# Performance work log

Hardware: AMD Instinct MI355X
Metric: run time of the kernel (lower is better)

## Reference

```python
import jax, jax.numpy as jnp
import numpy as np

N_TOTAL = 32768   # sphere points
N0 = 8192         # stage-0 nodes
N1 = 1024         # stage-1/2 nodes per branch
K = 8             # neighbors
C_IN, C_H = 128, 64
COS_T = 0.999     # NMS angular suppression threshold (~2.5 deg)
NEG = -1e30


def setup_inputs():
    key = jax.random.key(0)
    ks = jax.random.split(key, 32)
    f32 = jnp.float32
    def w(k, shape):
        return jax.random.normal(k, shape, f32) * 0.05
    feat_sphere = jax.random.normal(ks[0], (C_IN, N_TOTAL), f32)
    xyz = jax.random.normal(ks[1], (N_TOTAL, 3), f32)
    xyz = xyz / jnp.linalg.norm(xyz, axis=1, keepdims=True)
    inp = {"feat_sphere": feat_sphere, "xyz": xyz}
    for i, nm in enumerate(["0", "1", "2"]):
        inp["ws" + nm] = w(ks[2 + 2 * i], (C_H, C_IN))
        inp["bs" + nm] = w(ks[3 + 2 * i], (C_H,))
    for i, nm in enumerate(["0", "1", "2"]):
        b = 8 + 5 * i
        inp["dg" + nm + "_Wself"] = w(ks[b], (4, C_H, C_H))
        inp["dg" + nm + "_Wnb"] = w(ks[b + 1], (4, C_H, C_H))
        inp["dg" + nm + "_b"] = w(ks[b + 2], (4, C_H))
        inp["dg" + nm + "_head"] = w(ks[b + 3], (C_H,))
        inp["dg" + nm + "_hb"] = w(ks[b + 4], (1,))
    center0 = jnp.repeat(jnp.arange(N0, dtype=jnp.int32), K)
    nb0 = jax.random.randint(ks[24], (N0 * K,), 0, N0)
    inp["edge0"] = jnp.stack([center0, nb0])
    inp["ind0"] = jax.random.randint(ks[25], (N0,), 0, N_TOTAL)
    inp["ind1_scale"] = jax.random.randint(ks[26], (N_TOTAL, N1), 0, N_TOTAL)
    inp["ind2_scale"] = jax.random.randint(ks[27], (N_TOTAL, N1), 0, N_TOTAL)
    return inp


def _dgcn(x, center, neighbor, Wself, Wnb, bias, head, hb, n):
    # x: [n, C_H]; 4 graph-conv layers: self transform + mean-aggregated neighbor transform
    for i in range(Wself.shape[0]):
        agg = jax.ops.segment_sum(x[neighbor], center, num_segments=n) / K
        x = jax.nn.relu(x @ Wself[i] + agg @ Wnb[i] + bias[i])
    return x @ head + hb[0]  # [n] per-node score


def _nms3(scores, pts):
    # greedy sphere NMS, 3 peaks, suppress |dot| >= COS_T (antipodal-symmetric)
    idxs = []
    s = scores
    for _ in range(3):
        i = jnp.argmax(s)
        idxs.append(i)
        d = jnp.abs(pts @ pts[i])
        s = jnp.where(d >= COS_T, NEG, s)
    return jnp.stack(idxs)


def reference(feat_sphere, xyz, ws0, bs0, ws1, bs1, ws2, bs2,
              dg0_Wself, dg0_Wnb, dg0_b, dg0_head, dg0_hb,
              dg1_Wself, dg1_Wnb, dg1_b, dg1_head, dg1_hb,
              dg2_Wself, dg2_Wnb, dg2_b, dg2_head, dg2_hb,
              edge0, ind0, ind1_scale, ind2_scale):
    def sphere_feat(ind, W, b):
        # SPHERE gather + 1x1 conv (128->64): [S, C_H]
        return feat_sphere[:, ind].T @ W.T + b

    center = jnp.repeat(jnp.arange(N1, dtype=jnp.int32), K)

    # ---- stage 0 ----
    x0 = sphere_feat(ind0, ws0, bs0)                       # [N0, 64]
    s0 = _dgcn(x0, edge0[0], edge0[1], dg0_Wself, dg0_Wnb, dg0_b, dg0_head, dg0_hb, N0)
    xyz0 = xyz[ind0]
    idx1 = _nms3(s0, xyz0)                                 # [3]
    anchor1 = ind0[idx1]
    ind1 = ind1_scale[anchor1]                             # [3, N1]

    # ---- stage 1 ----
    xyz1 = xyz[ind1]                                       # [3, N1, 3]
    dis1 = jnp.abs(jnp.einsum('bnd,bmd->bnm', xyz1, xyz1))
    _, nb1 = jax.lax.top_k(dis1, K)                        # [3, N1, K]
    x1 = sphere_feat(ind1.reshape(-1), ws1, bs1).reshape(3, N1, C_H)
    s1 = jax.vmap(lambda xf, nb: _dgcn(xf, center, nb.reshape(-1),
                                       dg1_Wself, dg1_Wnb, dg1_b, dg1_head, dg1_hb, N1))(x1, nb1)
    idx2 = jnp.argmax(s1, axis=1)                          # [3]
    anchor2 = jnp.take_along_axis(ind1, idx2[:, None], axis=1).ravel()
    ind2 = ind2_scale[anchor2]                             # [3, N1]

    # ---- stage 2 ----
    xyz2 = xyz[ind2]
    dis2 = jnp.abs(jnp.einsum('bnd,bmd->bnm', xyz2, xyz2))
    _, nb2 = jax.lax.top_k(dis2, K)
    x2 = sphere_feat(ind2.reshape(-1), ws2, bs2).reshape(3, N1, C_H)
    s2 = jax.vmap(lambda xf, nb: _dgcn(xf, center, nb.reshape(-1),
                                       dg2_Wself, dg2_Wnb, dg2_b, dg2_head, dg2_hb, N1))(x2, nb2)

    return jnp.concatenate([jax.nn.sigmoid(s0), jax.nn.sigmoid(s1).ravel(), jax.nn.sigmoid(s2).ravel()])
```

## Files before the change

### kernel.cpp

```cpp
#include <hip/hip_runtime.h>
#include <math.h>

#define N_TOTAL 32768
#define N0 8192
#define N1 1024
#define KNB 8
#define C_IN 128
#define C_H 64
#define COS_T 0.999f
#define NEG_INF -1e30f
#define GRID 512
#define BLOCK 512
#define NACT 384
#define SLOT_DONE 0x7fffffffu

__device__ __forceinline__ void stc(float* p, float v) {
    __hip_atomic_store(p, v, __ATOMIC_RELAXED, __HIP_MEMORY_SCOPE_AGENT);
}
__device__ __forceinline__ void stci(int* p, int v) {
    __hip_atomic_store(p, v, __ATOMIC_RELAXED, __HIP_MEMORY_SCOPE_AGENT);
}
__device__ __forceinline__ float ldc(const float* p) {
    return __hip_atomic_load(p, __ATOMIC_RELAXED, __HIP_MEMORY_SCOPE_AGENT);
}

struct MegaParams {
    const float* feat;
    const float* xyz;
    const float* wsS[3];
    const float* bsS[3];
    const float* dgWs[3];
    const float* dgWn[3];
    const float* dgB[3];
    const float* dgH[3];
    const float* dgHb[3];
    const int* nb0;
    const int* ind0;
    const int* isc[2];
    float* out;
    float* xs0[4];
    float* xs1[4];
    float* xs2[4];
    float* s0;
    float* sbr;
    float* xyz0;
    float* featT;
    int* anchorA;
    int* anchorB;
    int* indb1; int* nbb1;
    int* indb2; int* nbb2;
    unsigned* slot;
    unsigned* flag;
    int tr;
    int actCoh;
};

__global__ void __launch_bounds__(BLOCK, 4) mega_kernel(MegaParams P) {
    const int blk = blockIdx.x;
    const int tid = threadIdx.x;
    const int w = tid >> 6;
    const int lane = tid & 63;

    __shared__ alignas(16) union {
        float tt[64][129];
        struct { float wt[C_H * 132]; float col[8][C_IN]; } sp;
        struct { float ws[C_H * 68]; float wn[C_H * 68];
                 float xw[8][C_H]; float aw[8][C_H]; } dg;
        struct { float sx[N1]; float sy[N1]; float sz[N1]; } tk;
        float sc[N0];
    } u;
    __shared__ float rv[BLOCK];
    __shared__ int ri[BLOCK];
    __shared__ float psel[3];

    auto BAR = [&](int e) {
        asm volatile("s_waitcnt vmcnt(0)" ::: "memory");
        __syncthreads();
        if (blk == 0) {
            if (tid > 0 && tid < GRID) {
                while (__hip_atomic_load(&P.slot[tid], __ATOMIC_RELAXED,
                                         __HIP_MEMORY_SCOPE_AGENT) < (unsigned)e)
                    __builtin_amdgcn_s_sleep(1);
            }
            __syncthreads();
            if (tid < 8)
                __hip_atomic_store(&P.flag[tid * 16], (unsigned)e, __ATOMIC_RELAXED,
                                   __HIP_MEMORY_SCOPE_AGENT);
            __syncthreads();
        } else {
            if (tid == 0) {
                __hip_atomic_store(&P.slot[blk], (unsigned)e, __ATOMIC_RELAXED,
                                   __HIP_MEMORY_SCOPE_AGENT);
                while (__hip_atomic_load(&P.flag[(blk & 7) * 16], __ATOMIC_RELAXED,
                                         __HIP_MEMORY_SCOPE_AGENT) < (unsigned)e)
                    __builtin_amdgcn_s_sleep(2);
            }
            __syncthreads();
        }
    };

    auto sphere = [&](int npb, const int* ind, const float* W, const float* bv,
                      float* xout) {
        __syncthreads();
        const float4* W4 = (const float4*)W;
        for (int i4 = tid; i4 < C_H * C_IN / 4; i4 += BLOCK) {
            int c = i4 >> 5, kg = i4 & 31;
            *(float4*)&u.sp.wt[c * 132 + kg * 4] = W4[i4];
        }
        __syncthreads();
        for (int it = 0; it < npb / 8; ++it) {
            int j = blk * npb + it * 8 + w;
            int p = ind[j];
            if (P.tr) {
                u.sp.col[w][lane]      = P.featT[(size_t)p * C_IN + lane];
                u.sp.col[w][lane + 64] = P.featT[(size_t)p * C_IN + lane + 64];
            } else {
                u.sp.col[w][lane]      = P.feat[(size_t)lane * N_TOTAL + p];
                u.sp.col[w][lane + 64] = P.feat[(size_t)(lane + 64) * N_TOTAL + p];
            }
            float acc = bv[lane];
#pragma unroll
            for (int k4 = 0; k4 < C_IN / 4; ++k4) {
                float4 cv = *(const float4*)&u.sp.col[w][k4 * 4];
                float4 wv = *(const float4*)&u.sp.wt[lane * 132 + k4 * 4];
                acc += cv.x * wv.x;
                acc += cv.y * wv.y;
                acc += cv.z * wv.z;
                acc += cv.w * wv.w;
            }
            stc(&xout[(size_t)j * C_H + lane], acc);
        }
    };

    auto dgcn = [&](int npb, const float* xin, const int* nbp,
                    const float* Wsl, const float* Wnl, const float* bias, int l,
                    float* xout, bool last, const float* head, const float* hb,
                    float* sdst, float* odst) {
        __syncthreads();
        const float* Ws_ = Wsl + l * C_H * C_H;
        const float* Wn_ = Wnl + l * C_H * C_H;
        for (int i = tid; i < C_H * C_H; i += BLOCK) {
            int k = i >> 6, c = i & 63;
            u.dg.ws[c * 68 + k] = Ws_[i];
            u.dg.wn[c * 68 + k] = Wn_[i];
        }
        __syncthreads();
        for (int ni = w; ni < npb; ni += 8) {
            int j = blk * npb + ni;
            float xv, a = 0.f;
            if (!P.actCoh) {
                xv = xin[(size_t)j * C_H + lane];
#pragma unroll
                for (int t = 0; t < KNB; ++t) {
                    int q = nbp[j * KNB + t];
                    a += xin[(size_t)q * C_H + lane];
                }
            } else {
                xv = ldc(&xin[(size_t)j * C_H + lane]);
#pragma unroll
                for (int t = 0; t < KNB; ++t) {
                    int q = nbp[j * KNB + t];
                    a += ldc(&xin[(size_t)q * C_H + lane]);
                }
            }
            u.dg.xw[w][lane] = xv;
            u.dg.aw[w][lane] = a * (1.0f / KNB);
            float acc = bias[l * C_H + lane];
#pragma unroll
            for (int k4 = 0; k4 < C_H / 4; ++k4) {
                float4 xv4 = *(const float4*)&u.dg.xw[w][k4 * 4];
                float4 av4 = *(const float4*)&u.dg.aw[w][k4 * 4];
                float4 wsv = *(const float4*)&u.dg.ws[lane * 68 + k4 * 4];
                float4 wnv = *(const float4*)&u.dg.wn[lane * 68 + k4 * 4];
                acc += xv4.x * wsv.x + av4.x * wnv.x;
                acc += xv4.y * wsv.y + av4.y * wnv.y;
                acc += xv4.z * wsv.z + av4.z * wnv.z;
                acc += xv4.w * wsv.w + av4.w * wnv.w;
            }
            acc = fmaxf(acc, 0.f);
            if (!last) {
                stc(&xout[(size_t)j * C_H + lane], acc);
            } else {
                float v = acc * head[lane];
#pragma unroll
                for (int off = 32; off > 0; off >>= 1) v += __shfl_down(v, off, 64);
                if (lane == 0) {
                    float s = v + hb[0];
                    if (sdst) stc(&sdst[j], s);
                    odst[j] = 1.f / (1.f + expf(-s));
                }
            }
        }
    };

    auto topk = [&](const int* isc, const int* anc, int* indb, int* nbb) {
        __syncthreads();
        const int b = blk >> 7;
        const int a = anc[b];
        const int* row = isc + (size_t)a * N1;
#pragma unroll
        for (int mm = 0; mm < 2; ++mm) {
            int m = mm * BLOCK + tid;
            int pp = row[m];
            u.tk.sx[m] = P.xyz[pp * 3 + 0];
            u.tk.sy[m] = P.xyz[pp * 3 + 1];
            u.tk.sz[m] = P.xyz[pp * 3 + 2];
        }
        if (tid < 8) {
            int grow = blk * 8 + tid;
            stci(&indb[grow], row[grow & (N1 - 1)]);
        }
        __syncthreads();
        {
            const int grow = blk * 8 + w;
            const int r = grow & (N1 - 1);
            float rx = u.tk.sx[r], ry = u.tk.sy[r], rz = u.tk.sz[r];
            unsigned long long k[16];
#pragma unroll
            for (int t = 0; t < 16; ++t) {
                int m = t * 64 + lane;
                float v = fabsf(rx * u.tk.sx[m] + ry * u.tk.sy[m] + rz * u.tk.sz[m]);
                k[t] = ((unsigned long long)__float_as_uint(v) << 32)
                     | (unsigned int)(0xFFFFFFFFu - (unsigned int)m);
            }
#pragma unroll
            for (int pass = 0; pass < KNB; ++pass) {
                unsigned long long lm = k[0];
#pragma unroll
                for (int t = 1; t < 16; ++t) lm = (k[t] > lm) ? k[t] : lm;
#pragma unroll
                for (int off = 1; off < 64; off <<= 1) {
                    unsigned long long o = __shfl_xor(lm, off, 64);
                    lm = (o > lm) ? o : lm;
                }
                if (lane == 0) {
                    int idx = (int)(0xFFFFFFFFu - (unsigned int)(lm & 0xFFFFFFFFull));
                    stci(&nbb[grow * KNB + pass], b * N1 + idx);
                }
#pragma unroll
                for (int t = 0; t < 16; ++t) if (k[t] == lm) k[t] = 0;
            }
        }
        asm volatile("s_waitcnt vmcnt(0)" ::: "memory");
        __syncthreads();
    };

    if (P.tr) {
        const int g0 = blk * 64;
        const int col = tid & 63, rowH = tid >> 6;
        for (int c0 = 0; c0 < C_IN; c0 += 8) {
            int c = c0 + rowH;
            u.tt[col][c] = P.feat[(size_t)c * N_TOTAL + g0 + col];
        }
        __syncthreads();
        for (int i = tid; i < 64 * C_IN; i += BLOCK) {
            int cc = i >> 7, c = i & 127;
            stc(&P.featT[(size_t)(g0 + cc) * C_IN + c], u.tt[cc][c]);
        }
    }
    if (tid < 16) {
        int j = blk * 16 + tid;
        int p = P.ind0[j];
        stc(&P.xyz0[j * 3 + 0], P.xyz[p * 3 + 0]);
        stc(&P.xyz0[j * 3 + 1], P.xyz[p * 3 + 1]);
        stc(&P.xyz0[j * 3 + 2], P.xyz[p * 3 + 2]);
    }
    BAR(1);

    sphere(16, P.ind0, P.wsS[0], P.bsS[0], P.xs0[0]);
    BAR(2);
    dgcn(16, P.xs0[0], P.nb0, P.dgWs[0], P.dgWn[0], P.dgB[0], 0, P.xs0[1], false, nullptr, nullptr, nullptr, nullptr);
    BAR(3);
    dgcn(16, P.xs0[1], P.nb0, P.dgWs[0], P.dgWn[0], P.dgB[0], 1, P.xs0[2], false, nullptr, nullptr, nullptr, nullptr);
    BAR(4);
    dgcn(16, P.xs0[2], P.nb0, P.dgWs[0], P.dgWn[0], P.dgB[0], 2, P.xs0[3], false, nullptr, nullptr, nullptr, nullptr);
    BAR(5);
    dgcn(16, P.xs0[3], P.nb0, P.dgWs[0], P.dgWn[0], P.dgB[0], 3, nullptr, true,
         P.dgH[0], P.dgHb[0], P.s0, P.out);

    if (blk >= NACT) {
        asm volatile("s_waitcnt vmcnt(0)" ::: "memory");
        __syncthreads();
        if (tid == 0)
            __hip_atomic_store(&P.slot[blk], SLOT_DONE, __ATOMIC_RELAXED,
                               __HIP_MEMORY_SCOPE_AGENT);
        return;
    }
    BAR(6);

    if (blk == 0) {
        for (int jj = tid; jj < N0; jj += BLOCK) u.sc[jj] = P.s0[jj];
        __syncthreads();
        for (int it = 0; it < 3; ++it) {
            float bv = -INFINITY; int bi = 0x7fffffff;
            for (int jj = tid; jj < N0; jj += BLOCK) {
                float v = u.sc[jj];
                if (v > bv) { bv = v; bi = jj; }
            }
            rv[tid] = bv; ri[tid] = bi;
            __syncthreads();
            for (int sft = BLOCK / 2; sft > 0; sft >>= 1) {
                if (tid < sft) {
                    float v2 = rv[tid + sft]; int i2 = ri[tid + sft];
                    if (v2 > rv[tid] || (v2 == rv[tid] && i2 < ri[tid])) {
                        rv[tid] = v2; ri[tid] = i2;
                    }
                }
                __syncthreads();
            }
            int sel = ri[0];
            if (tid == 0) {
                stci(&P.anchorA[it], P.ind0[sel]);
                psel[0] = P.xyz0[sel * 3 + 0];
                psel[1] = P.xyz0[sel * 3 + 1];
                psel[2] = P.xyz0[sel * 3 + 2];
            }
            __syncthreads();
            float px = psel[0], py = psel[1], pz = psel[2];
            for (int jj = tid; jj < N0; jj += BLOCK) {
                float d = fabsf(P.xyz0[jj * 3 + 0] * px + P.xyz0[jj * 3 + 1] * py
                              + P.xyz0[jj * 3 + 2] * pz);
                if (d >= COS_T) u.sc[jj] = NEG_INF;
            }
            __syncthreads();
        }
    }
    BAR(7);

    for (int st = 1; st <= 2; ++st) {
        float* const* xb = (st == 1) ? P.xs1 : P.xs2;
        int* indb = (st == 1) ? P.indb1 : P.indb2;
        int* nbb  = (st == 1) ? P.nbb1  : P.nbb2;
        const int* anc = (st == 1) ? P.anchorA : P.anchorB;
        const int ep = (st == 1) ? 7 : 13;

        topk(P.isc[st - 1], anc, indb, nbb);
        sphere(8, indb, P.wsS[st], P.bsS[st], xb[0]);
        BAR(ep + 1);
        dgcn(8, xb[0], nbb, P.dgWs[st], P.dgWn[st], P.dgB[st], 0, xb[1], false, nullptr, nullptr, nullptr, nullptr);
        BAR(ep + 2);
        dgcn(8, xb[1], nbb, P.dgWs[st], P.dgWn[st], P.dgB[st], 1, xb[2], false, nullptr, nullptr, nullptr, nullptr);
        BAR(ep + 3);
        dgcn(8, xb[2], nbb, P.dgWs[st], P.dgWn[st], P.dgB[st], 2, xb[3], false, nullptr, nullptr, nullptr, nullptr);
        BAR(ep + 4);
        dgcn(8, xb[3], nbb, P.dgWs[st], P.dgWn[st], P.dgB[st], 3, nullptr, true,
             P.dgH[st], P.dgHb[st], (st == 1) ? P.sbr : nullptr,
             P.out + N0 + (st - 1) * 3 * N1);
        if (st == 1) {
            BAR(12);
            if (blk < 3) {
                float bv = -INFINITY; int bi = 0x7fffffff;
                for (int m = tid; m < N1; m += BLOCK) {
                    float v = P.sbr[blk * N1 + m];
                    if (v > bv) { bv = v; bi = m; }
                }
                rv[tid] = bv; ri[tid] = bi;
                __syncthreads();
                for (int sft = BLOCK / 2; sft > 0; sft >>= 1) {
                    if (tid < sft) {
                        float v2 = rv[tid + sft]; int i2 = ri[tid + sft];
                        if (v2 > rv[tid] || (v2 == rv[tid] && i2 < ri[tid])) {
                            rv[tid] = v2; ri[tid] = i2;
                        }
                    }
                    __syncthreads();
                }
                if (tid == 0) stci(&P.anchorB[blk], P.indb1[blk * N1 + ri[0]]);
            }
            BAR(13);
        }
    }
}

extern "C" void kernel_launch(void* const* d_in, const int* in_sizes, int n_in,
                              void* d_out, int out_size, void* d_ws, size_t ws_size,
                              hipStream_t stream) {
    MegaParams hp;
    hp.feat = (const float*)d_in[0];
    hp.xyz  = (const float*)d_in[1];
    hp.wsS[0] = (const float*)d_in[2];  hp.bsS[0] = (const float*)d_in[3];
    hp.wsS[1] = (const float*)d_in[4];  hp.bsS[1] = (const float*)d_in[5];
    hp.wsS[2] = (const float*)d_in[6];  hp.bsS[2] = (const float*)d_in[7];
    hp.dgWs[0] = (const float*)d_in[8];  hp.dgWn[0] = (const float*)d_in[9];
    hp.dgB[0]  = (const float*)d_in[10]; hp.dgH[0]  = (const float*)d_in[11];
    hp.dgHb[0] = (const float*)d_in[12];
    hp.dgWs[1] = (const float*)d_in[13]; hp.dgWn[1] = (const float*)d_in[14];
    hp.dgB[1]  = (const float*)d_in[15]; hp.dgH[1]  = (const float*)d_in[16];
    hp.dgHb[1] = (const float*)d_in[17];
    hp.dgWs[2] = (const float*)d_in[18]; hp.dgWn[2] = (const float*)d_in[19];
    hp.dgB[2]  = (const float*)d_in[20]; hp.dgH[2]  = (const float*)d_in[21];
    hp.dgHb[2] = (const float*)d_in[22];
    const int* edge0 = (const int*)d_in[23];
    hp.nb0  = edge0 + N0 * KNB;
    hp.ind0 = (const int*)d_in[24];
    hp.isc[0] = (const int*)d_in[25];
    hp.isc[1] = (const int*)d_in[26];
    hp.out = (float*)d_out;

    float* f = (float*)d_ws;
    size_t o = 0;
    auto takeF = [&](size_t n) { float* p = f + o; o += n; return p; };

    hp.s0   = takeF(N0);
    hp.sbr  = takeF(3 * N1);
    hp.xyz0 = takeF((size_t)N0 * 3);
    o = (o + 63) & ~(size_t)63;
    hp.anchorA = (int*)takeF(64);
    hp.anchorB = (int*)takeF(64);
    hp.indb1 = (int*)takeF(3 * N1);
    hp.nbb1  = (int*)takeF(3 * N1 * KNB);
    hp.indb2 = (int*)takeF(3 * N1);
    hp.nbb2  = (int*)takeF(3 * N1 * KNB);
    o = (o + 63) & ~(size_t)63;
    hp.slot = (unsigned*)takeF(GRID);
    hp.flag = (unsigned*)takeF(8 * 16);
    unsigned* ctrBase = hp.slot;

    size_t needFast = (o + 4 * (size_t)N0 * C_H + 8 * (size_t)(3 * N1) * C_H) * sizeof(float);
    if (ws_size >= needFast) {
        hp.actCoh = 0;
        for (int i = 0; i < 4; ++i) hp.xs0[i] = takeF((size_t)N0 * C_H);
        for (int i = 0; i < 4; ++i) hp.xs1[i] = takeF((size_t)(3 * N1) * C_H);
        for (int i = 0; i < 4; ++i) hp.xs2[i] = takeF((size_t)(3 * N1) * C_H);
    } else {
        hp.actCoh = 1;
        float* xA = takeF((size_t)N0 * C_H);
        float* xB = takeF((size_t)N0 * C_H);
        for (int i = 0; i < 4; ++i) {
            hp.xs0[i] = (i & 1) ? xB : xA;
            hp.xs1[i] = (i & 1) ? xB : xA;
            hp.xs2[i] = (i & 1) ? xB : xA;
        }
    }

    size_t needTr = (o + (size_t)N_TOTAL * C_IN) * sizeof(float);
    if (ws_size >= needTr) {
        hp.tr = 1;
        hp.featT = takeF((size_t)N_TOTAL * C_IN);
    } else {
        hp.tr = 0;
        hp.featT = nullptr;
    }

    hipMemsetAsync((void*)ctrBase, 0, (GRID + 8 * 16) * sizeof(unsigned), stream);
    mega_kernel<<<dim3(GRID), dim3(BLOCK), 0, stream>>>(hp);
}
```

Baseline: 189.2 us.

## Process two nodes per wave and remap stage-1/2 work across all blocks

Each wave now handles two nodes at once in the sphere projection and graph-conv layers. This doubles the independent gathers in flight and reuses each LDS weight read for two dot products. For stages 1 and 2 the work map changes: blocks are interleaved by branch (blk&7), only 3 of every 8 blocks do work, each handling 16 rows, and all blocks stay in the grid barriers instead of 128 blocks retiring early. The intent is to hide gather latency and improve ILP, at the cost of more registers and idle blocks still taking part in barrier synchronisation.

After: 244.1 us. 29.1% more time.

```diff
diff --git a/kernel.cpp b/kernel.cpp
--- a/kernel.cpp
+++ b/kernel.cpp
@@ -11,8 +11,6 @@
 #define NEG_INF -1e30f
 #define GRID 512
 #define BLOCK 512
-#define NACT 384
-#define SLOT_DONE 0x7fffffffu
 
 __device__ __forceinline__ void stc(float* p, float v) {
     __hip_atomic_store(p, v, __ATOMIC_RELAXED, __HIP_MEMORY_SCOPE_AGENT);
@@ -63,9 +61,9 @@
 
     __shared__ alignas(16) union {
         float tt[64][129];
-        struct { float wt[C_H * 132]; float col[8][C_IN]; } sp;
+        struct { float wt[C_H * 132]; float col[16][C_IN]; } sp;
         struct { float ws[C_H * 68]; float wn[C_H * 68];
-                 float xw[8][C_H]; float aw[8][C_H]; } dg;
+                 float xw[16][C_H]; float aw[16][C_H]; } dg;
         struct { float sx[N1]; float sy[N1]; float sz[N1]; } tk;
         float sc[N0];
     } u;
@@ -99,7 +97,7 @@
         }
     };
 
-    auto sphere = [&](int npb, const int* ind, const float* W, const float* bv,
+    auto sphere = [&](int jb, const int* ind, const float* W, const float* bv,
                       float* xout) {
         __syncthreads();
         const float4* W4 = (const float4*)W;
@@ -108,31 +106,35 @@
             *(float4*)&u.sp.wt[c * 132 + kg * 4] = W4[i4];
         }
         __syncthreads();
-        for (int it = 0; it < npb / 8; ++it) {
-            int j = blk * npb + it * 8 + w;
-            int p = ind[j];
-            if (P.tr) {
-                u.sp.col[w][lane]      = P.featT[(size_t)p * C_IN + lane];
-                u.sp.col[w][lane + 64] = P.featT[(size_t)p * C_IN + lane + 64];
-            } else {
-                u.sp.col[w][lane]      = P.feat[(size_t)lane * N_TOTAL + p];
-                u.sp.col[w][lane + 64] = P.feat[(size_t)(lane + 64) * N_TOTAL + p];
-            }
-            float acc = bv[lane];
-#pragma unroll
-            for (int k4 = 0; k4 < C_IN / 4; ++k4) {
-                float4 cv = *(const float4*)&u.sp.col[w][k4 * 4];
-                float4 wv = *(const float4*)&u.sp.wt[lane * 132 + k4 * 4];
-                acc += cv.x * wv.x;
-                acc += cv.y * wv.y;
-                acc += cv.z * wv.z;
-                acc += cv.w * wv.w;
-            }
-            stc(&xout[(size_t)j * C_H + lane], acc);
-        }
+        const int j0 = jb + w, j1 = jb + 8 + w;
+        const int p0 = ind[j0], p1 = ind[j1];
+        if (P.tr) {
+            u.sp.col[2 * w + 0][lane]      = P.featT[(size_t)p0 * C_IN + lane];
+            u.sp.col[2 * w + 0][lane + 64] = P.featT[(size_t)p0 * C_IN + lane + 64];
+            u.sp.col[2 * w + 1][lane]      = P.featT[(size_t)p1 * C_IN + lane];
+            u.sp.col[2 * w + 1][lane + 64] = P.featT[(size_t)p1 * C_IN + lane + 64];
+        } else {
+            u.sp.col[2 * w + 0][lane]      = P.feat[(size_t)lane * N_TOTAL + p0];
+            u.sp.col[2 * w + 0][lane + 64] = P.feat[(size_t)(lane + 64) * N_TOTAL + p0];
+            u.sp.col[2 * w + 1][lane]      = P.feat[(size_t)lane * N_TOTAL + p1];
+            u.sp.col[2 * w + 1][lane + 64] = P.feat[(size_t)(lane + 64) * N_TOTAL + p1];
+        }
+        float acc0 = bv[lane], acc1 = acc0;
+#pragma unroll
+        for (int k4 = 0; k4 < C_IN / 4; ++k4) {
+            float4 c0 = *(const float4*)&u.sp.col[2 * w + 0][k4 * 4];
+            float4 c1 = *(const float4*)&u.sp.col[2 * w + 1][k4 * 4];
+            float4 wv = *(const float4*)&u.sp.wt[lane * 132 + k4 * 4];
+            acc0 += c0.x * wv.x; acc1 += c1.x * wv.x;
+            acc0 += c0.y * wv.y; acc1 += c1.y * wv.y;
+            acc0 += c0.z * wv.z; acc1 += c1.z * wv.z;
+            acc0 += c0.w * wv.w; acc1 += c1.w * wv.w;
+        }
+        stc(&xout[(size_t)j0 * C_H + lane], acc0);
+        stc(&xout[(size_t)j1 * C_H + lane], acc1);
     };
 
-    auto dgcn = [&](int npb, const float* xin, const int* nbp,
+    auto dgcn = [&](int jb, const float* xin, const int* nbp,
                     const float* Wsl, const float* Wnl, const float* bias, int l,
                     float* xout, bool last, const float* head, const float* hb,
                     float* sdst, float* odst) {
@@ -145,58 +147,77 @@
             u.dg.wn[c * 68 + k] = Wn_[i];
         }
         __syncthreads();
-        for (int ni = w; ni < npb; ni += 8) {
-            int j = blk * npb + ni;
-            float xv, a = 0.f;
-            if (!P.actCoh) {
-                xv = xin[(size_t)j * C_H + lane];
-#pragma unroll
-                for (int t = 0; t < KNB; ++t) {
-                    int q = nbp[j * KNB + t];
-                    a += xin[(size_t)q * C_H + lane];
-                }
-            } else {
-                xv = ldc(&xin[(size_t)j * C_H + lane]);
-#pragma unroll
-                for (int t = 0; t < KNB; ++t) {
-                    int q = nbp[j * KNB + t];
-                    a += ldc(&xin[(size_t)q * C_H + lane]);
-                }
-            }
-            u.dg.xw[w][lane] = xv;
-            u.dg.aw[w][lane] = a * (1.0f / KNB);
-            float acc = bias[l * C_H + lane];
-#pragma unroll
-            for (int k4 = 0; k4 < C_H / 4; ++k4) {
-                float4 xv4 = *(const float4*)&u.dg.xw[w][k4 * 4];
-                float4 av4 = *(const float4*)&u.dg.aw[w][k4 * 4];
-                float4 wsv = *(const float4*)&u.dg.ws[lane * 68 + k4 * 4];
-                float4 wnv = *(const float4*)&u.dg.wn[lane * 68 + k4 * 4];
-                acc += xv4.x * wsv.x + av4.x * wnv.x;
-                acc += xv4.y * wsv.y + av4.y * wnv.y;
-                acc += xv4.z * wsv.z + av4.z * wnv.z;
-                acc += xv4.w * wsv.w + av4.w * wnv.w;
-            }
-            acc = fmaxf(acc, 0.f);
-            if (!last) {
-                stc(&xout[(size_t)j * C_H + lane], acc);
-            } else {
-                float v = acc * head[lane];
-#pragma unroll
-                for (int off = 32; off > 0; off >>= 1) v += __shfl_down(v, off, 64);
-                if (lane == 0) {
-                    float s = v + hb[0];
-                    if (sdst) stc(&sdst[j], s);
-                    odst[j] = 1.f / (1.f + expf(-s));
-                }
+        const int j0 = jb + w, j1 = jb + 8 + w;
+        float xv0, xv1, n0[KNB], n1[KNB];
+        int q0[KNB], q1[KNB];
+#pragma unroll
+        for (int t = 0; t < KNB; ++t) q0[t] = nbp[j0 * KNB + t];
+#pragma unroll
+        for (int t = 0; t < KNB; ++t) q1[t] = nbp[j1 * KNB + t];
+        if (!P.actCoh) {
+            xv0 = xin[(size_t)j0 * C_H + lane];
+            xv1 = xin[(size_t)j1 * C_H + lane];
+#pragma unroll
+            for (int t = 0; t < KNB; ++t) n0[t] = xin[(size_t)q0[t] * C_H + lane];
+#pragma unroll
+            for (int t = 0; t < KNB; ++t) n1[t] = xin[(size_t)q1[t] * C_H + lane];
+        } else {
+            xv0 = ldc(&xin[(size_t)j0 * C_H + lane]);
+            xv1 = ldc(&xin[(size_t)j1 * C_H + lane]);
+#pragma unroll
+            for (int t = 0; t < KNB; ++t) n0[t] = ldc(&xin[(size_t)q0[t] * C_H + lane]);
+#pragma unroll
+            for (int t = 0; t < KNB; ++t) n1[t] = ldc(&xin[(size_t)q1[t] * C_H + lane]);
+        }
+        float a0 = 0.f, a1 = 0.f;
+#pragma unroll
+        for (int t = 0; t < KNB; ++t) a0 += n0[t];
+#pragma unroll
+        for (int t = 0; t < KNB; ++t) a1 += n1[t];
+        u.dg.xw[2 * w + 0][lane] = xv0;
+        u.dg.xw[2 * w + 1][lane] = xv1;
+        u.dg.aw[2 * w + 0][lane] = a0 * (1.0f / KNB);
+        u.dg.aw[2 * w + 1][lane] = a1 * (1.0f / KNB);
+        float acc0 = bias[l * C_H + lane], acc1 = acc0;
+#pragma unroll
+        for (int k4 = 0; k4 < C_H / 4; ++k4) {
+            float4 x0 = *(const float4*)&u.dg.xw[2 * w + 0][k4 * 4];
+            float4 x1 = *(const float4*)&u.dg.xw[2 * w + 1][k4 * 4];
+            float4 g0 = *(const float4*)&u.dg.aw[2 * w + 0][k4 * 4];
+            float4 g1 = *(const float4*)&u.dg.aw[2 * w + 1][k4 * 4];
+            float4 wsv = *(const float4*)&u.dg.ws[lane * 68 + k4 * 4];
+            float4 wnv = *(const float4*)&u.dg.wn[lane * 68 + k4 * 4];
+            acc0 += x0.x * wsv.x + g0.x * wnv.x;  acc1 += x1.x * wsv.x + g1.x * wnv.x;
+            acc0 += x0.y * wsv.y + g0.y * wnv.y;  acc1 += x1.y * wsv.y + g1.y * wnv.y;
+            acc0 += x0.z * wsv.z + g0.z * wnv.z;  acc1 += x1.z * wsv.z + g1.z * wnv.z;
+            acc0 += x0.w * wsv.w + g0.w * wnv.w;  acc1 += x1.w * wsv.w + g1.w * wnv.w;
+        }
+        acc0 = fmaxf(acc0, 0.f);
+        acc1 = fmaxf(acc1, 0.f);
+        if (!last) {
+            stc(&xout[(size_t)j0 * C_H + lane], acc0);
+            stc(&xout[(size_t)j1 * C_H + lane], acc1);
+        } else {
+            float v0 = acc0 * head[lane];
+            float v1 = acc1 * head[lane];
+#pragma unroll
+            for (int off = 32; off > 0; off >>= 1) {
+                v0 += __shfl_down(v0, off, 64);
+                v1 += __shfl_down(v1, off, 64);
+            }
+            if (lane == 0) {
+                float s0v = v0 + hb[0], s1v = v1 + hb[0];
+                if (sdst) { stc(&sdst[j0], s0v); stc(&sdst[j1], s1v); }
+                odst[j0] = 1.f / (1.f + expf(-s0v));
+                odst[j1] = 1.f / (1.f + expf(-s1v));
             }
         }
     };
 
-    auto topk = [&](const int* isc, const int* anc, int* indb, int* nbb) {
-        __syncthreads();
-        const int b = blk >> 7;
-        const int a = anc[b];
+    auto topk = [&](const int* isc, const int* anc, int* indb, int* nbb,
+                    int br, int sl) {
+        __syncthreads();
+        const int a = anc[br];
         const int* row = isc + (size_t)a * N1;
 #pragma unroll
         for (int mm = 0; mm < 2; ++mm) {
@@ -206,14 +227,15 @@
             u.tk.sy[m] = P.xyz[pp * 3 + 1];
             u.tk.sz[m] = P.xyz[pp * 3 + 2];
         }
-        if (tid < 8) {
-            int grow = blk * 8 + tid;
-            stci(&indb[grow], row[grow & (N1 - 1)]);
-        }
-        __syncthreads();
-        {
-            const int grow = blk * 8 + w;
-            const int r = grow & (N1 - 1);
+        if (tid < 16) {
+            int r = sl * 16 + tid;
+            stci(&indb[br * N1 + r], row[r]);
+        }
+        __syncthreads();
+#pragma unroll
+        for (int rr = 0; rr < 2; ++rr) {
+            const int r = sl * 16 + rr * 8 + w;
+            const int grow = br * N1 + r;
             float rx = u.tk.sx[r], ry = u.tk.sy[r], rz = u.tk.sz[r];
             unsigned long long k[16];
 #pragma unroll
@@ -235,7 +257,7 @@
                 }
                 if (lane == 0) {
                     int idx = (int)(0xFFFFFFFFu - (unsigned int)(lm & 0xFFFFFFFFull));
-                    stci(&nbb[grow * KNB + pass], b * N1 + idx);
+                    stci(&nbb[grow * KNB + pass], br * N1 + idx);
                 }
 #pragma unroll
                 for (int t = 0; t < 16; ++t) if (k[t] == lm) k[t] = 0;
@@ -267,25 +289,17 @@
     }
     BAR(1);
 
-    sphere(16, P.ind0, P.wsS[0], P.bsS[0], P.xs0[0]);
+    const int jb0 = blk * 16;
+    sphere(jb0, P.ind0, P.wsS[0], P.bsS[0], P.xs0[0]);
     BAR(2);
-    dgcn(16, P.xs0[0], P.nb0, P.dgWs[0], P.dgWn[0], P.dgB[0], 0, P.xs0[1], false, nullptr, nullptr, nullptr, nullptr);
+    dgcn(jb0, P.xs0[0], P.nb0, P.dgWs[0], P.dgWn[0], P.dgB[0], 0, P.xs0[1], false, nullptr, nullptr, nullptr, nullptr);
     BAR(3);
-    dgcn(16, P.xs0[1], P.nb0, P.dgWs[0], P.dgWn[0], P.dgB[0], 1, P.xs0[2], false, nullptr, nullptr, nullptr, nullptr);
+    dgcn(jb0, P.xs0[1], P.nb0, P.dgWs[0], P.dgWn[0], P.dgB[0], 1, P.xs0[2], false, nullptr, nullptr, nullptr, nullptr);
     BAR(4);
-    dgcn(16, P.xs0[2], P.nb0, P.dgWs[0], P.dgWn[0], P.dgB[0], 2, P.xs0[3], false, nullptr, nullptr, nullptr, nullptr);
+    dgcn(jb0, P.xs0[2], P.nb0, P.dgWs[0], P.dgWn[0], P.dgB[0], 2, P.xs0[3], false, nullptr, nullptr, nullptr, nullptr);
     BAR(5);
-    dgcn(16, P.xs0[3], P.nb0, P.dgWs[0], P.dgWn[0], P.dgB[0], 3, nullptr, true,
+    dgcn(jb0, P.xs0[3], P.nb0, P.dgWs[0], P.dgWn[0], P.dgB[0], 3, nullptr, true,
          P.dgH[0], P.dgHb[0], P.s0, P.out);
-
-    if (blk >= NACT) {
-        asm volatile("s_waitcnt vmcnt(0)" ::: "memory");
-        __syncthreads();
-        if (tid == 0)
-            __hip_atomic_store(&P.slot[blk], SLOT_DONE, __ATOMIC_RELAXED,
-                               __HIP_MEMORY_SCOPE_AGENT);
-        return;
-    }
     BAR(6);
 
     if (blk == 0) {
@@ -327,6 +341,11 @@
     }
     BAR(7);
 
+    const int br = blk & 7;
+    const int sl = blk >> 3;
+    const bool act12 = (br < 3);
+    const int jb12 = br * N1 + sl * 16;
+
     for (int st = 1; st <= 2; ++st) {
         float* const* xb = (st == 1) ? P.xs1 : P.xs2;
         int* indb = (st == 1) ? P.indb1 : P.indb2;
@@ -334,18 +353,20 @@
         const int* anc = (st == 1) ? P.anchorA : P.anchorB;
         const int ep = (st == 1) ? 7 : 13;
 
-        topk(P.isc[st - 1], anc, indb, nbb);
-        sphere(8, indb, P.wsS[st], P.bsS[st], xb[0]);
+        if (act12) {
+            topk(P.isc[st - 1], anc, indb, nbb, br, sl);
+            sphere(jb12, indb, P.wsS[st], P.bsS[st], xb[0]);
+        }
         BAR(ep + 1);
-        dgcn(8, xb[0], nbb, P.dgWs[st], P.dgWn[st], P.dgB[st], 0, xb[1], false, nullptr, nullptr, nullptr, nullptr);
+        if (act12) dgcn(jb12, xb[0], nbb, P.dgWs[st], P.dgWn[st], P.dgB[st], 0, xb[1], false, nullptr, nullptr, nullptr, nullptr);
         BAR(ep + 2);
-        dgcn(8, xb[1], nbb, P.dgWs[st], P.dgWn[st], P.dgB[st], 1, xb[2], false, nullptr, nullptr, nullptr, nullptr);
+        if (act12) dgcn(jb12, xb[1], nbb, P.dgWs[st], P.dgWn[st], P.dgB[st], 1, xb[2], false, nullptr, nullptr, nullptr, nullptr);
         BAR(ep + 3);
-        dgcn(8, xb[2], nbb, P.dgWs[st], P.dgWn[st], P.dgB[st], 2, xb[3], false, nullptr, nullptr, nullptr, nullptr);
+        if (act12) dgcn(jb12, xb[2], nbb, P.dgWs[st], P.dgWn[st], P.dgB[st], 2, xb[3], false, nullptr, nullptr, nullptr, nullptr);
         BAR(ep + 4);
-        dgcn(8, xb[3], nbb, P.dgWs[st], P.dgWn[st], P.dgB[st], 3, nullptr, true,
-             P.dgH[st], P.dgHb[st], (st == 1) ? P.sbr : nullptr,
-             P.out + N0 + (st - 1) * 3 * N1);
+        if (act12) dgcn(jb12, xb[3], nbb, P.dgWs[st], P.dgWn[st], P.dgB[st], 3, nullptr, true,
+                        P.dgH[st], P.dgHb[st], (st == 1) ? P.sbr : nullptr,
+                        P.out + N0 + (st - 1) * 3 * N1);
         if (st == 1) {
             BAR(12);
             if (blk < 3) {
```
